# Optimization experiments

Measured on AMD Instinct MI355X. Metric: run time of the kernel, lower is better.

## Reference

```python
import jax, jax.numpy as jnp
import numpy as np


def _fake_quant(x, clip_val, level):
    """PACT-style non-negative fake quantization with STE on rounding.

    clamp to [0, clip_val], quantize to `level` uniform levels, dequantize.
    """
    c = clip_val.reshape(())
    scale = c / (level - 1)
    xc = jnp.clip(x, 0.0, c)
    q = jnp.round(xc / scale) * scale
    # straight-through: forward value is q, gradient flows through xc
    return xc + jax.lax.stop_gradient(q - xc)


def setup_inputs() -> dict:
    key = jax.random.key(0)
    k1, k2 = jax.random.split(key)
    B, M, K, N = 8, 4096, 64, 4096
    x1 = jax.random.uniform(k1, (B, M, K), dtype=jnp.float32)
    x2 = jax.random.uniform(k2, (B, K, N), dtype=jnp.float32)
    clip_val1 = jnp.ones((1,), dtype=jnp.float32)
    clip_val2 = jnp.ones((1,), dtype=jnp.float32)
    return {"x1": x1, "x2": x2, "clip_val1": clip_val1,
            "clip_val2": clip_val2, "level": 256}


def reference(x1, x2, clip_val1, clip_val2, level):
    q1 = _fake_quant(x1, clip_val1, level)  # [B, M, K]
    q2 = _fake_quant(x2, clip_val2, level)  # [B, K, N]
    return jnp.matmul(q1, q2)               # [B, M, N]
```

## Files before the change

kernel.cpp:

```cpp
#include <hip/hip_runtime.h>
#include <hip/hip_bf16.h>


#define BATCH 8
#define MDIM 4096
#define KDIM 64
#define NDIM 4096

typedef __attribute__((ext_vector_type(4))) unsigned short u16x4;
typedef __attribute__((ext_vector_type(8))) short s16x8;
typedef __attribute__((ext_vector_type(4))) float f32x4;

__device__ __forceinline__ unsigned short qcode(float x, float c, float inv) {
    float xc = fminf(fmaxf(x, 0.0f), c);
    float k = rintf(xc * inv);
    return (unsigned short)(__float_as_uint(k) >> 16);
}

__global__ void quantA_k(const float* __restrict__ x, unsigned short* __restrict__ q,
                         const float* __restrict__ clip, const int* __restrict__ level,
                         int n4) {
    float c = clip[0];
    float inv = (float)(level[0] - 1) / c;
    int i = blockIdx.x * 256 + threadIdx.x;
    if (i >= n4) return;
    float4 v = ((const float4*)x)[i];
    u16x4 o;
    o[0] = qcode(v.x, c, inv);
    o[1] = qcode(v.y, c, inv);
    o[2] = qcode(v.z, c, inv);
    o[3] = qcode(v.w, c, inv);
    ((u16x4*)q)[i] = o;
}

__global__ void quantB_t(const float* __restrict__ x, unsigned short* __restrict__ q,
                         const float* __restrict__ clip, const int* __restrict__ level) {
    __shared__ unsigned short T[64 * 68];
    int b = blockIdx.y;
    int n0 = blockIdx.x * 64;
    float c = clip[0];
    float inv = (float)(level[0] - 1) / c;
    int t = threadIdx.x;

    const float* src = x + (size_t)b * KDIM * NDIM + n0;
#pragma unroll
    for (int it = 0; it < 4; ++it) {
        int qi = t + it * 256;
        int k = qi >> 4, c4 = qi & 15;
        float4 v = *(const float4*)(src + (size_t)k * NDIM + c4 * 4);
        u16x4 o;
        o[0] = qcode(v.x, c, inv);
        o[1] = qcode(v.y, c, inv);
        o[2] = qcode(v.z, c, inv);
        o[3] = qcode(v.w, c, inv);
        *(u16x4*)&T[k * 68 + c4 * 4] = o;
    }
    __syncthreads();

    unsigned short* dst = q + ((size_t)b * NDIM + n0) * KDIM;
#pragma unroll
    for (int it = 0; it < 4; ++it) {
        int qi = t + it * 256;
        int n = qi >> 4, c4 = qi & 15;
        u16x4 o;
        o[0] = T[(c4 * 4 + 0) * 68 + n];
        o[1] = T[(c4 * 4 + 1) * 68 + n];
        o[2] = T[(c4 * 4 + 2) * 68 + n];
        o[3] = T[(c4 * 4 + 3) * 68 + n];
        *(u16x4*)(dst + (size_t)n * KDIM + c4 * 4) = o;
    }
}

__global__ __launch_bounds__(256)
void gemm_q(const unsigned short* __restrict__ qA, const unsigned short* __restrict__ qBt,
            const float* __restrict__ c1p, const float* __restrict__ c2p,
            const int* __restrict__ lvp, float* __restrict__ out) {
    __shared__ unsigned short As[128 * 64];
    __shared__ unsigned short Bs[128 * 64];

    const int b = blockIdx.z, mt = blockIdx.y, nt = blockIdx.x;
    const int t = threadIdx.x;

    const unsigned short* gA = qA + ((size_t)b * MDIM + mt * 128) * KDIM;
    const unsigned short* gB = qBt + ((size_t)b * NDIM + nt * 128) * KDIM;

#pragma unroll
    for (int it = 0; it < 4; ++it) {
        int qi = t + it * 256;
        int row = qi >> 3, c8 = qi & 7;
        s16x8 va = *(const s16x8*)(gA + (size_t)row * KDIM + c8 * 8);
        s16x8 vb = *(const s16x8*)(gB + (size_t)row * KDIM + c8 * 8);
        int off = (row * 128 + c8 * 16) ^ ((row & 7) << 4);
        *(s16x8*)((char*)As + off) = va;
        *(s16x8*)((char*)Bs + off) = vb;
    }
    __syncthreads();

    const int lane = t & 63, w = t >> 6;
    const int wr = (w >> 1) * 64, wc = (w & 1) * 64;
    const int r16 = lane & 15, kq = lane >> 4;

    f32x4 acc[4][4] = {};
#pragma unroll
    for (int ks = 0; ks < 2; ++ks) {
        const int kb = ks * 64 + kq * 16;
        s16x8 a[4], bf[4];
#pragma unroll
        for (int mf = 0; mf < 4; ++mf) {
            int row = wr + mf * 16 + r16;
            int off = (row * 128 + kb) ^ ((row & 7) << 4);
            a[mf] = *(const s16x8*)((const char*)As + off);
        }
#pragma unroll
        for (int nf = 0; nf < 4; ++nf) {
            int row = wc + nf * 16 + r16;
            int off = (row * 128 + kb) ^ ((row & 7) << 4);
            bf[nf] = *(const s16x8*)((const char*)Bs + off);
        }
#pragma unroll
        for (int mf = 0; mf < 4; ++mf)
#pragma unroll
            for (int nf = 0; nf < 4; ++nf)
                acc[mf][nf] = __builtin_amdgcn_mfma_f32_16x16x32_bf16(
                    a[mf], bf[nf], acc[mf][nf], 0, 0, 0);
    }

    float c1 = c1p[0], c2 = c2p[0];
    float lvm1 = (float)(lvp[0] - 1);
    float s = (c1 / lvm1) * (c2 / lvm1);

    size_t obase = (size_t)b * MDIM * NDIM;
    int m0 = mt * 128 + wr, n0 = nt * 128 + wc;
#pragma unroll
    for (int mf = 0; mf < 4; ++mf) {
#pragma unroll
        for (int i = 0; i < 4; ++i) {
            int m = m0 + mf * 16 + kq * 4 + i;
            float* orow = out + obase + (size_t)m * NDIM + n0 + r16;
#pragma unroll
            for (int nf = 0; nf < 4; ++nf)
                orow[nf * 16] = acc[mf][nf][i] * s;
        }
    }
}

extern "C" void kernel_launch(void* const* d_in, const int* in_sizes, int n_in,
                              void* d_out, int out_size, void* d_ws, size_t ws_size,
                              hipStream_t stream) {
    const float* x1 = (const float*)d_in[0];
    const float* x2 = (const float*)d_in[1];
    const float* c1 = (const float*)d_in[2];
    const float* c2 = (const float*)d_in[3];
    const int* lv   = (const int*)d_in[4];
    float* out = (float*)d_out;

    unsigned short* qA = (unsigned short*)d_ws;
    unsigned short* qB = qA + (size_t)BATCH * MDIM * KDIM;

    quantA_k<<<(BATCH * MDIM * KDIM / 4 + 255) / 256, 256, 0, stream>>>(
        x1, qA, c1, lv, BATCH * MDIM * KDIM / 4);
    quantB_t<<<dim3(NDIM / 64, BATCH), 256, 0, stream>>>(x2, qB, c2, lv);
    gemm_q<<<dim3(NDIM / 128, MDIM / 128, BATCH), 256, 0, stream>>>(
        qA, qB, c1, c2, lv, out);
}
```

Baseline: 110.5 us.

## Fuse fake-quantization of both operands into the GEMM kernel

Drops the two separate quantization kernels and the workspace round trip. The GEMM now loads fp32 x1 and x2 tiles directly, quantizes them to bf16 codes in registers, and transposes the B tile through an extra shared-memory buffer before the MFMA loop. This removes two launches and the write and re-read of the quantized intermediates. In exchange, each tile's fp32 input is re-read and re-quantized by every block sharing it, which doubles input bytes per block and adds LDS use and an extra barrier.

Measured after the change: 137.3 us. 1.24x slower.

```diff
diff --git a/kernel.cpp b/kernel.cpp
--- a/kernel.cpp
+++ b/kernel.cpp
@@ -6,6 +6,7 @@
 #define MDIM 4096
 #define KDIM 64
 #define NDIM 4096
+#define TMPS 132
 
 typedef __attribute__((ext_vector_type(4))) unsigned short u16x4;
 typedef __attribute__((ext_vector_type(8))) short s16x8;
@@ -17,82 +18,74 @@
     return (unsigned short)(__float_as_uint(k) >> 16);
 }
 
-__global__ void quantA_k(const float* __restrict__ x, unsigned short* __restrict__ q,
-                         const float* __restrict__ clip, const int* __restrict__ level,
-                         int n4) {
-    float c = clip[0];
-    float inv = (float)(level[0] - 1) / c;
-    int i = blockIdx.x * 256 + threadIdx.x;
-    if (i >= n4) return;
-    float4 v = ((const float4*)x)[i];
-    u16x4 o;
-    o[0] = qcode(v.x, c, inv);
-    o[1] = qcode(v.y, c, inv);
-    o[2] = qcode(v.z, c, inv);
-    o[3] = qcode(v.w, c, inv);
-    ((u16x4*)q)[i] = o;
-}
-
-__global__ void quantB_t(const float* __restrict__ x, unsigned short* __restrict__ q,
-                         const float* __restrict__ clip, const int* __restrict__ level) {
-    __shared__ unsigned short T[64 * 68];
-    int b = blockIdx.y;
-    int n0 = blockIdx.x * 64;
-    float c = clip[0];
-    float inv = (float)(level[0] - 1) / c;
-    int t = threadIdx.x;
-
-    const float* src = x + (size_t)b * KDIM * NDIM + n0;
-#pragma unroll
-    for (int it = 0; it < 4; ++it) {
-        int qi = t + it * 256;
-        int k = qi >> 4, c4 = qi & 15;
-        float4 v = *(const float4*)(src + (size_t)k * NDIM + c4 * 4);
-        u16x4 o;
-        o[0] = qcode(v.x, c, inv);
-        o[1] = qcode(v.y, c, inv);
-        o[2] = qcode(v.z, c, inv);
-        o[3] = qcode(v.w, c, inv);
-        *(u16x4*)&T[k * 68 + c4 * 4] = o;
-    }
-    __syncthreads();
-
-    unsigned short* dst = q + ((size_t)b * NDIM + n0) * KDIM;
-#pragma unroll
-    for (int it = 0; it < 4; ++it) {
-        int qi = t + it * 256;
-        int n = qi >> 4, c4 = qi & 15;
-        u16x4 o;
-        o[0] = T[(c4 * 4 + 0) * 68 + n];
-        o[1] = T[(c4 * 4 + 1) * 68 + n];
-        o[2] = T[(c4 * 4 + 2) * 68 + n];
-        o[3] = T[(c4 * 4 + 3) * 68 + n];
-        *(u16x4*)(dst + (size_t)n * KDIM + c4 * 4) = o;
-    }
+__device__ __forceinline__ s16x8 qpack(float4 v0, float4 v1, float c, float inv) {
+    s16x8 o;
+    o[0] = (short)qcode(v0.x, c, inv);
+    o[1] = (short)qcode(v0.y, c, inv);
+    o[2] = (short)qcode(v0.z, c, inv);
+    o[3] = (short)qcode(v0.w, c, inv);
+    o[4] = (short)qcode(v1.x, c, inv);
+    o[5] = (short)qcode(v1.y, c, inv);
+    o[6] = (short)qcode(v1.z, c, inv);
+    o[7] = (short)qcode(v1.w, c, inv);
+    return o;
 }
 
 __global__ __launch_bounds__(256)
-void gemm_q(const unsigned short* __restrict__ qA, const unsigned short* __restrict__ qBt,
-            const float* __restrict__ c1p, const float* __restrict__ c2p,
-            const int* __restrict__ lvp, float* __restrict__ out) {
+void fq_gemm(const float* __restrict__ x1, const float* __restrict__ x2,
+             const float* __restrict__ c1p, const float* __restrict__ c2p,
+             const int* __restrict__ lvp, float* __restrict__ out) {
     __shared__ unsigned short As[128 * 64];
     __shared__ unsigned short Bs[128 * 64];
+    __shared__ unsigned short Tmp[64 * TMPS];
 
     const int b = blockIdx.z, mt = blockIdx.y, nt = blockIdx.x;
     const int t = threadIdx.x;
 
-    const unsigned short* gA = qA + ((size_t)b * MDIM + mt * 128) * KDIM;
-    const unsigned short* gB = qBt + ((size_t)b * NDIM + nt * 128) * KDIM;
+    const float c1 = c1p[0], c2 = c2p[0];
+    const float lvm1 = (float)(lvp[0] - 1);
+    const float inv1 = lvm1 / c1, inv2 = lvm1 / c2;
+
+    const float* gA = x1 + ((size_t)b * MDIM + mt * 128) * KDIM;
+#pragma unroll
+    for (int it = 0; it < 4; ++it) {
+        int qi = t + it * 256;
+        int m = qi >> 3, c8 = qi & 7;
+        const float* p = gA + (size_t)m * KDIM + c8 * 8;
+        float4 v0 = *(const float4*)p;
+        float4 v1 = *(const float4*)(p + 4);
+        int off = (m * 128 + c8 * 16) ^ ((m & 7) << 4);
+        *(s16x8*)((char*)As + off) = qpack(v0, v1, c1, inv1);
+    }
+
+    const float* gB = x2 + (size_t)b * KDIM * NDIM + nt * 128;
+#pragma unroll
+    for (int it = 0; it < 4; ++it) {
+        int qi = t + it * 256;
+        int k = qi >> 4, c8 = qi & 15;
+        const float* p = gB + (size_t)k * NDIM + c8 * 8;
+        float4 v0 = *(const float4*)p;
+        float4 v1 = *(const float4*)(p + 4);
+        s16x8 o = qpack(v0, v1, c2, inv2);
+        char* q = (char*)Tmp + (size_t)k * (TMPS * 2) + c8 * 16;
+        u16x4 lo, hi;
+        lo[0] = o[0]; lo[1] = o[1]; lo[2] = o[2]; lo[3] = o[3];
+        hi[0] = o[4]; hi[1] = o[5]; hi[2] = o[6]; hi[3] = o[7];
+        *(u16x4*)q = lo;
+        *(u16x4*)(q + 8) = hi;
+    }
+    __syncthreads();
 
 #pragma unroll
     for (int it = 0; it < 4; ++it) {
         int qi = t + it * 256;
-        int row = qi >> 3, c8 = qi & 7;
-        s16x8 va = *(const s16x8*)(gA + (size_t)row * KDIM + c8 * 8);
-        s16x8 vb = *(const s16x8*)(gB + (size_t)row * KDIM + c8 * 8);
-        int off = (row * 128 + c8 * 16) ^ ((row & 7) << 4);
-        *(s16x8*)((char*)As + off) = va;
-        *(s16x8*)((char*)Bs + off) = vb;
+        int n = qi >> 3, k8 = qi & 7, k0 = k8 * 8;
+        s16x8 o;
+#pragma unroll
+        for (int j = 0; j < 8; ++j)
+            o[j] = (short)Tmp[(size_t)(k0 + j) * TMPS + n];
+        int off = (n * 128 + k8 * 16) ^ ((n & 7) << 4);
+        *(s16x8*)((char*)Bs + off) = o;
     }
     __syncthreads();
 
@@ -125,10 +118,7 @@
                     a[mf], bf[nf], acc[mf][nf], 0, 0, 0);
     }
 
-    float c1 = c1p[0], c2 = c2p[0];
-    float lvm1 = (float)(lvp[0] - 1);
-    float s = (c1 / lvm1) * (c2 / lvm1);
-
+    const float s = (c1 / lvm1) * (c2 / lvm1);
     size_t obase = (size_t)b * MDIM * NDIM;
     int m0 = mt * 128 + wr, n0 = nt * 128 + wc;
 #pragma unroll
@@ -154,12 +144,6 @@
     const int* lv   = (const int*)d_in[4];
     float* out = (float*)d_out;
 
-    unsigned short* qA = (unsigned short*)d_ws;
-    unsigned short* qB = qA + (size_t)BATCH * MDIM * KDIM;
-
-    quantA_k<<<(BATCH * MDIM * KDIM / 4 + 255) / 256, 256, 0, stream>>>(
-        x1, qA, c1, lv, BATCH * MDIM * KDIM / 4);
-    quantB_t<<<dim3(NDIM / 64, BATCH), 256, 0, stream>>>(x2, qB, c2, lv);
-    gemm_q<<<dim3(NDIM / 128, MDIM / 128, BATCH), 256, 0, stream>>>(
-        qA, qB, c1, c2, lv, out);
+    fq_gemm<<<dim3(NDIM / 128, MDIM / 128, BATCH), 256, 0, stream>>>(
+        x1, x2, c1, c2, lv, out);
 }
```

## Merge quant kernels, drop GEMM LDS staging, swap MFMA operands for vector stores

Applied to the files above, without the earlier changes.

The two quantization kernels become one launch, with block-index ranges selecting the A path or the transposed-B path, which saves a kernel launch. The GEMM no longer stages tiles in shared memory; each lane loads its MFMA fragments straight from global memory and the barrier is gone. The MFMA operands are swapped so each lane holds four consecutive output columns, letting the epilogue write float4 stores instead of scalar ones. The direct global loads rely on L2/L1 for reuse across waves, and because the kernel is dominated by writing the large output, the store vectorization is the main intended gain.

Result: slower. 133.4 us (+20.7%).

```diff
diff --git a/kernel.cpp b/kernel.cpp
--- a/kernel.cpp
+++ b/kernel.cpp
@@ -17,32 +17,35 @@
     return (unsigned short)(__float_as_uint(k) >> 16);
 }
 
-__global__ void quantA_k(const float* __restrict__ x, unsigned short* __restrict__ q,
-                         const float* __restrict__ clip, const int* __restrict__ level,
-                         int n4) {
-    float c = clip[0];
-    float inv = (float)(level[0] - 1) / c;
-    int i = blockIdx.x * 256 + threadIdx.x;
-    if (i >= n4) return;
-    float4 v = ((const float4*)x)[i];
-    u16x4 o;
-    o[0] = qcode(v.x, c, inv);
-    o[1] = qcode(v.y, c, inv);
-    o[2] = qcode(v.z, c, inv);
-    o[3] = qcode(v.w, c, inv);
-    ((u16x4*)q)[i] = o;
-}
+#define QA_BLOCKS 2048
 
-__global__ void quantB_t(const float* __restrict__ x, unsigned short* __restrict__ q,
-                         const float* __restrict__ clip, const int* __restrict__ level) {
+__global__ void quant_both(const float* __restrict__ x1, const float* __restrict__ x2,
+                           unsigned short* __restrict__ qA, unsigned short* __restrict__ qBt,
+                           const float* __restrict__ c1p, const float* __restrict__ c2p,
+                           const int* __restrict__ lvp) {
     __shared__ unsigned short T[64 * 68];
-    int b = blockIdx.y;
-    int n0 = blockIdx.x * 64;
-    float c = clip[0];
-    float inv = (float)(level[0] - 1) / c;
-    int t = threadIdx.x;
+    const int t = threadIdx.x;
+    const float lvm1 = (float)(lvp[0] - 1);
 
-    const float* src = x + (size_t)b * KDIM * NDIM + n0;
+    if (blockIdx.x < QA_BLOCKS) {
+        const float c = c1p[0], inv = lvm1 / c;
+        int i = blockIdx.x * 256 + t;
+        float4 v = ((const float4*)x1)[i];
+        u16x4 o;
+        o[0] = qcode(v.x, c, inv);
+        o[1] = qcode(v.y, c, inv);
+        o[2] = qcode(v.z, c, inv);
+        o[3] = qcode(v.w, c, inv);
+        ((u16x4*)qA)[i] = o;
+        return;
+    }
+
+    const float c = c2p[0], inv = lvm1 / c;
+    int bi = blockIdx.x - QA_BLOCKS;
+    int b = bi >> 6;
+    int n0 = (bi & 63) * 64;
+
+    const float* src = x2 + (size_t)b * KDIM * NDIM + n0;
 #pragma unroll
     for (int it = 0; it < 4; ++it) {
         int qi = t + it * 256;
@@ -57,7 +60,7 @@
     }
     __syncthreads();
 
-    unsigned short* dst = q + ((size_t)b * NDIM + n0) * KDIM;
+    unsigned short* dst = qBt + ((size_t)b * NDIM + n0) * KDIM;
 #pragma unroll
     for (int it = 0; it < 4; ++it) {
         int qi = t + it * 256;
@@ -75,71 +78,54 @@
 void gemm_q(const unsigned short* __restrict__ qA, const unsigned short* __restrict__ qBt,
             const float* __restrict__ c1p, const float* __restrict__ c2p,
             const int* __restrict__ lvp, float* __restrict__ out) {
-    __shared__ unsigned short As[128 * 64];
-    __shared__ unsigned short Bs[128 * 64];
-
     const int b = blockIdx.z, mt = blockIdx.y, nt = blockIdx.x;
     const int t = threadIdx.x;
-
-    const unsigned short* gA = qA + ((size_t)b * MDIM + mt * 128) * KDIM;
-    const unsigned short* gB = qBt + ((size_t)b * NDIM + nt * 128) * KDIM;
-
-#pragma unroll
-    for (int it = 0; it < 4; ++it) {
-        int qi = t + it * 256;
-        int row = qi >> 3, c8 = qi & 7;
-        s16x8 va = *(const s16x8*)(gA + (size_t)row * KDIM + c8 * 8);
-        s16x8 vb = *(const s16x8*)(gB + (size_t)row * KDIM + c8 * 8);
-        int off = (row * 128 + c8 * 16) ^ ((row & 7) << 4);
-        *(s16x8*)((char*)As + off) = va;
-        *(s16x8*)((char*)Bs + off) = vb;
-    }
-    __syncthreads();
-
     const int lane = t & 63, w = t >> 6;
     const int wr = (w >> 1) * 64, wc = (w & 1) * 64;
     const int r16 = lane & 15, kq = lane >> 4;
 
+    const unsigned short* pA =
+        qA + ((size_t)b * MDIM + mt * 128 + wr + r16) * KDIM + kq * 8;
+    const unsigned short* pB =
+        qBt + ((size_t)b * NDIM + nt * 128 + wc + r16) * KDIM + kq * 8;
+
     f32x4 acc[4][4] = {};
 #pragma unroll
     for (int ks = 0; ks < 2; ++ks) {
-        const int kb = ks * 64 + kq * 16;
         s16x8 a[4], bf[4];
 #pragma unroll
-        for (int mf = 0; mf < 4; ++mf) {
-            int row = wr + mf * 16 + r16;
-            int off = (row * 128 + kb) ^ ((row & 7) << 4);
-            a[mf] = *(const s16x8*)((const char*)As + off);
-        }
+        for (int mf = 0; mf < 4; ++mf)
+            a[mf] = *(const s16x8*)(pA + mf * 16 * KDIM + ks * 32);
 #pragma unroll
-        for (int nf = 0; nf < 4; ++nf) {
-            int row = wc + nf * 16 + r16;
-            int off = (row * 128 + kb) ^ ((row & 7) << 4);
-            bf[nf] = *(const s16x8*)((const char*)Bs + off);
-        }
+        for (int nf = 0; nf < 4; ++nf)
+            bf[nf] = *(const s16x8*)(pB + nf * 16 * KDIM + ks * 32);
 #pragma unroll
         for (int mf = 0; mf < 4; ++mf)
 #pragma unroll
             for (int nf = 0; nf < 4; ++nf)
                 acc[mf][nf] = __builtin_amdgcn_mfma_f32_16x16x32_bf16(
-                    a[mf], bf[nf], acc[mf][nf], 0, 0, 0);
+                    bf[nf], a[mf], acc[mf][nf], 0, 0, 0);
     }
 
-    float c1 = c1p[0], c2 = c2p[0];
-    float lvm1 = (float)(lvp[0] - 1);
-    float s = (c1 / lvm1) * (c2 / lvm1);
+    const float c1 = c1p[0], c2 = c2p[0];
+    const float lvm1 = (float)(lvp[0] - 1);
+    const float s = (c1 / lvm1) * (c2 / lvm1);
 
     size_t obase = (size_t)b * MDIM * NDIM;
-    int m0 = mt * 128 + wr, n0 = nt * 128 + wc;
+    const int m0 = mt * 128 + wr, n0 = nt * 128 + wc;
 #pragma unroll
     for (int mf = 0; mf < 4; ++mf) {
+        int m = m0 + mf * 16 + r16;
+        float* orow = out + obase + (size_t)m * NDIM;
 #pragma unroll
-        for (int i = 0; i < 4; ++i) {
-            int m = m0 + mf * 16 + kq * 4 + i;
-            float* orow = out + obase + (size_t)m * NDIM + n0 + r16;
-#pragma unroll
-            for (int nf = 0; nf < 4; ++nf)
-                orow[nf * 16] = acc[mf][nf][i] * s;
+        for (int nf = 0; nf < 4; ++nf) {
+            int nb = n0 + nf * 16 + kq * 4;
+            float4 v;
+            v.x = acc[mf][nf][0] * s;
+            v.y = acc[mf][nf][1] * s;
+            v.z = acc[mf][nf][2] * s;
+            v.w = acc[mf][nf][3] * s;
+            *(float4*)(orow + nb) = v;
         }
     }
 }
@@ -157,9 +143,8 @@
     unsigned short* qA = (unsigned short*)d_ws;
     unsigned short* qB = qA + (size_t)BATCH * MDIM * KDIM;
 
-    quantA_k<<<(BATCH * MDIM * KDIM / 4 + 255) / 256, 256, 0, stream>>>(
-        x1, qA, c1, lv, BATCH * MDIM * KDIM / 4);
-    quantB_t<<<dim3(NDIM / 64, BATCH), 256, 0, stream>>>(x2, qB, c2, lv);
+    quant_both<<<QA_BLOCKS + BATCH * (NDIM / 64), 256, 0, stream>>>(
+        x1, x2, qA, qB, c1, c2, lv);
     gemm_q<<<dim3(NDIM / 128, MDIM / 128, BATCH), 256, 0, stream>>>(
         qA, qB, c1, c2, lv, out);
 }
```
